# Optimization experiments

Measured on AMD Instinct MI355X. Metric: run time of the kernel, lower is better.

Reference implementation:

```python
import jax, jax.numpy as jnp
import numpy as np

HEAD_DIM = 128
PROJ_DIM = 64


def setup_inputs() -> dict:
    key = jax.random.key(0)
    kq, kk, kv, kr = jax.random.split(key, 4)
    B, H, NQ, NKV = 1, 16, 2048, 4096
    Q = jax.random.normal(kq, (B, H, NQ, HEAD_DIM), dtype=jnp.float32)
    K = jax.random.normal(kk, (B, H, NKV, HEAD_DIM), dtype=jnp.float32)
    V = jax.random.normal(kv, (B, H, NKV, HEAD_DIM), dtype=jnp.float32)
    # R ~ N(0,1) / sqrt(proj_dim), as in the torch __init__
    R = jax.random.normal(kr, (HEAD_DIM, PROJ_DIM), dtype=jnp.float32) / (PROJ_DIM ** 0.5)
    return {"Q": Q, "K": K, "V": V, "R": R}


def reference(Q, K, V, R):
    proj_dim = R.shape[-1]
    scale = 1.0 / (proj_dim ** 0.5)
    # Project Q and K into the random-projection space: [B,H,N,proj_dim]
    Q_proj = jnp.einsum('bhnd,dp->bhnp', Q, R)
    K_proj = jnp.einsum('bhmd,dp->bhmp', K, R)
    # scores: [B,H,NQ,NKV]
    scores = jnp.einsum('bhnp,bhmp->bhnm', Q_proj, K_proj) * scale
    weights = jax.nn.softmax(scores, axis=-1)
    # output: [B,H,NQ,head_dim]
    return jnp.einsum('bhnm,bhmd->bhnd', weights, V)
```

## Files before the change

kernel.cpp:

```cpp
#include <hip/hip_runtime.h>

#define HEADS 16
#define NQ    2048
#define NKV   4096
#define DH    128
#define PDIM  64

typedef __bf16 bf16_t;
typedef bf16_t bf16x8 __attribute__((ext_vector_type(8)));
typedef bf16_t bf16x4 __attribute__((ext_vector_type(4)));
typedef bf16_t bf16x2 __attribute__((ext_vector_type(2)));
typedef float  f32x4  __attribute__((ext_vector_type(4)));
typedef float  f32x16 __attribute__((ext_vector_type(16)));
typedef int    i32x4  __attribute__((ext_vector_type(4)));

typedef __attribute__((address_space(3))) unsigned int       lds_u32;
typedef __attribute__((address_space(1))) const unsigned int glb_u32;

__device__ __forceinline__ void dma16(const void* g, void* l) {
  __builtin_amdgcn_global_load_lds((glb_u32*)g, (lds_u32*)l, 16, 0, 0);
}

__global__ __launch_bounds__(256) void prep_kernel(
    const float* __restrict__ Q, const float* __restrict__ K,
    const float* __restrict__ V, const float* __restrict__ R,
    bf16_t* __restrict__ Qp, bf16_t* __restrict__ Kp, bf16_t* __restrict__ Vt)
{
  __shared__ float  sF[64 * 132];
  __shared__ bf16_t sY[4][16 * 72];
  const int tid = threadIdx.x;
  const int bid = blockIdx.x;

  const int isQ = (bid < 512);
  const int isK = (bid >= 512) && (bid < 1536);

  const float* src;
  long row0;
  if (isQ)      { src = Q; row0 = (long)bid * 64; }
  else if (isK) { src = K; row0 = (long)(bid - 512) * 64; }
  else          { src = V; row0 = (long)(bid - 1536) * 64; }
  const float* tp = src + row0 * DH;
#pragma unroll
  for (int rep = 0; rep < 8; ++rep) {
    const int slot = tid + rep * 256;
    const int j = slot >> 5, c4 = (slot & 31) * 4;
    f32x4 v = *(const f32x4*)(tp + j * DH + c4);
    *(f32x4*)(&sF[j * 132 + c4]) = v;
  }
  __syncthreads();

  if (!isQ && !isK) {
    const int vb = bid - 1536;
    const int h = vb >> 6, jt = vb & 63;
    bf16_t* op = Vt + (long)h * DH * NKV + jt * 64;
#pragma unroll
    for (int rep = 0; rep < 4; ++rep) {
      const int slot = tid + rep * 256;
      const int d = slot >> 3, j8 = (slot & 7) * 8;
      bf16x8 w;
#pragma unroll
      for (int jj = 0; jj < 8; ++jj) w[jj] = (bf16_t)sF[(j8 + jj) * 132 + d];
      *(bf16x8*)(op + (long)d * NKV + j8) = w;
    }
    return;
  }

  const int wave = tid >> 6, lane = tid & 63;
  const int n16  = lane & 15, quad = lane >> 4;
  const float scale = isQ ? 0.18033688011112042f : 1.0f;
  bf16_t* Y = isQ ? Qp : Kp;

  bf16x8 bfr[4][4];
#pragma unroll
  for (int nt = 0; nt < 4; ++nt) {
    const int n = nt * 16 + n16;
#pragma unroll
    for (int kk = 0; kk < 4; ++kk) {
      const int k0 = kk * 32 + quad * 8;
      bf16x8 b;
#pragma unroll
      for (int j = 0; j < 8; ++j) b[j] = (bf16_t)R[(k0 + j) * PDIM + n];
      bfr[nt][kk] = b;
    }
  }

  const int arow = wave * 16 + n16;
  bf16x8 a[4];
#pragma unroll
  for (int kk = 0; kk < 4; ++kk) {
    const int k0 = kk * 32 + quad * 8;
    f32x4 x0 = *(const f32x4*)(&sF[arow * 132 + k0]);
    f32x4 x1 = *(const f32x4*)(&sF[arow * 132 + k0 + 4]);
    bf16x8 av;
#pragma unroll
    for (int j = 0; j < 4; ++j) { av[j] = (bf16_t)(x0[j] * scale); av[4 + j] = (bf16_t)(x1[j] * scale); }
    a[kk] = av;
  }

  bf16_t* sy = sY[wave];
#pragma unroll
  for (int nt = 0; nt < 4; ++nt) {
    f32x4 acc = {0.f, 0.f, 0.f, 0.f};
#pragma unroll
    for (int kk = 0; kk < 4; ++kk)
      acc = __builtin_amdgcn_mfma_f32_16x16x32_bf16(a[kk], bfr[nt][kk], acc, 0, 0, 0);
#pragma unroll
    for (int r = 0; r < 4; ++r)
      sy[(quad * 4 + r) * 72 + nt * 16 + n16] = (bf16_t)acc[r];
  }
  const long xrow = row0 + wave * 16;
  const int row = lane >> 2, cg = lane & 3;
  bf16x8 w0 = *(const bf16x8*)(&sy[row * 72 + cg * 16]);
  bf16x8 w1 = *(const bf16x8*)(&sy[row * 72 + cg * 16 + 8]);
  *(bf16x8*)(Y + (xrow + row) * PDIM + cg * 16)     = w0;
  *(bf16x8*)(Y + (xrow + row) * PDIM + cg * 16 + 8) = w1;
}

__global__ __launch_bounds__(128, 2) void flash_kernel(
    const bf16_t* __restrict__ Qp, const bf16_t* __restrict__ Kp,
    const bf16_t* __restrict__ Vt, bf16_t* __restrict__ Opart,
    float* __restrict__ Lpart, float* __restrict__ Out,
    int splits, int iters)
{
  __shared__ char smem[24576];
  bf16_t* sK = (bf16_t*)smem;
  bf16_t* sV = (bf16_t*)(smem + 8192);

  const int tid  = threadIdx.x;
  const int wave = tid >> 6, lane = tid & 63;
  const int l31  = lane & 31, h = lane >> 5;

  const int head = blockIdx.x & 15;
  const int qt   = (blockIdx.x >> 4) & 15;
  const int sp   = blockIdx.x >> 8;

  const int qbase = qt * 128 + wave * 64;
  const int kv0   = sp * (64 * iters);

  bf16x8 qf[2][4];
#pragma unroll
  for (int qsub = 0; qsub < 2; ++qsub)
#pragma unroll
    for (int k = 0; k < 4; ++k)
      qf[qsub][k] = *(const bf16x8*)(Qp + ((long)head * NQ + qbase + qsub * 32 + l31) * PDIM
                                     + k * 16 + h * 8);

  f32x16 o[2][4] = {};
  float rsum[2] = {0.f, 0.f};

  const bf16_t* kpH = Kp + (long)head * NKV * PDIM;
  const bf16_t* vtH = Vt + (long)head * DH * NKV;

  const int sw = ((lane & 7) ^ ((lane >> 3) & 7)) * 8;
  const int r8 = lane >> 3;

  for (int t = 0; t < iters; ++t) {
    const int kvb = kv0 + t * 64;
    __syncthreads();
    if (wave == 0) {
#pragma unroll
      for (int i = 0; i < 8; ++i)
        dma16(kpH + (long)(kvb + i * 8 + r8) * PDIM + sw, smem + i * 1024);
#pragma unroll
      for (int i = 0; i < 4; ++i)
        dma16(vtH + (long)(i * 8 + r8) * NKV + kvb + sw, smem + 8192 + i * 1024);
    } else {
#pragma unroll
      for (int i = 4; i < 16; ++i)
        dma16(vtH + (long)(i * 8 + r8) * NKV + kvb + sw, smem + 8192 + i * 1024);
    }
    __syncthreads();

#pragma unroll
    for (int s = 0; s < 2; ++s) {
      int bfr[2][2][4];
#pragma unroll
      for (int qsub = 0; qsub < 2; ++qsub) {
        f32x16 sc = {};
        const int r = s * 32 + l31;
#pragma unroll
        for (int k = 0; k < 4; ++k) {
          const int c = 2 * k + h;
          const bf16x8 a = *(const bf16x8*)(sK + r * 64 + ((c ^ (r & 7)) * 8));
          sc = __builtin_amdgcn_mfma_f32_32x32x16_bf16(a, qf[qsub][k], sc, 0, 0, 0);
        }
        int pk[4][2];
#pragma unroll
        for (int rg = 0; rg < 4; ++rg) {
          const float p0 = __builtin_amdgcn_exp2f(sc[rg * 4 + 0]);
          const float p1 = __builtin_amdgcn_exp2f(sc[rg * 4 + 1]);
          const float p2 = __builtin_amdgcn_exp2f(sc[rg * 4 + 2]);
          const float p3 = __builtin_amdgcn_exp2f(sc[rg * 4 + 3]);
          rsum[qsub] += (p0 + p1) + (p2 + p3);
          union { bf16x2 v; int i; } u0, u1;
          u0.v = bf16x2{(bf16_t)p0, (bf16_t)p1};
          u1.v = bf16x2{(bf16_t)p2, (bf16_t)p3};
          pk[rg][0] = u0.i; pk[rg][1] = u1.i;
        }
#pragma unroll
        for (int cl = 0; cl < 2; ++cl) {
          const int e00 = __shfl_xor(pk[2 * cl][0], 32);
          const int e01 = __shfl_xor(pk[2 * cl][1], 32);
          const int e10 = __shfl_xor(pk[2 * cl + 1][0], 32);
          const int e11 = __shfl_xor(pk[2 * cl + 1][1], 32);
          bfr[qsub][cl][0] = h ? e10 : pk[2 * cl][0];
          bfr[qsub][cl][1] = h ? e11 : pk[2 * cl][1];
          bfr[qsub][cl][2] = h ? pk[2 * cl + 1][0] : e00;
          bfr[qsub][cl][3] = h ? pk[2 * cl + 1][1] : e01;
        }
      }
#pragma unroll
      for (int dsub = 0; dsub < 4; ++dsub) {
        const int r = dsub * 32 + l31;
#pragma unroll
        for (int cl = 0; cl < 2; ++cl) {
          const int c = 2 * (2 * s + cl) + h;
          const bf16x8 va = *(const bf16x8*)(sV + r * 64 + ((c ^ (r & 7)) * 8));
#pragma unroll
          for (int qsub = 0; qsub < 2; ++qsub) {
            union { i32x4 i; bf16x8 v; } pb;
            pb.i = i32x4{bfr[qsub][cl][0], bfr[qsub][cl][1],
                         bfr[qsub][cl][2], bfr[qsub][cl][3]};
            o[qsub][dsub] = __builtin_amdgcn_mfma_f32_32x32x16_bf16(va, pb.v, o[qsub][dsub], 0, 0, 0);
          }
        }
      }
    }
  }

  __syncthreads();
  bf16_t* myT = (bf16_t*)(smem + wave * 8704);
#pragma unroll
  for (int qsub = 0; qsub < 2; ++qsub) {
    const float lsum = rsum[qsub] + __shfl_xor(rsum[qsub], 32);
    const float scale = (splits > 1) ? 1.0f : (1.0f / lsum);
#pragma unroll
    for (int dsub = 0; dsub < 4; ++dsub)
#pragma unroll
      for (int rg = 0; rg < 4; ++rg) {
        bf16x4 w = { (bf16_t)(o[qsub][dsub][rg * 4 + 0] * scale),
                     (bf16_t)(o[qsub][dsub][rg * 4 + 1] * scale),
                     (bf16_t)(o[qsub][dsub][rg * 4 + 2] * scale),
                     (bf16_t)(o[qsub][dsub][rg * 4 + 3] * scale) };
        *(bf16x4*)(myT + l31 * 136 + dsub * 32 + rg * 8 + h * 4) = w;
      }
    const int qglob = qbase + qsub * 32;
#pragma unroll
    for (int j = 0; j < 8; ++j) {
      const int ql = j * 4 + (lane >> 4);
      bf16x8 v = *(const bf16x8*)(myT + ql * 136 + (lane & 15) * 8);
      if (splits > 1) {
        *(bf16x8*)(Opart + (((long)sp * HEADS + head) * NQ + qglob + ql) * DH + (lane & 15) * 8) = v;
      } else {
        float* op = Out + ((long)head * NQ + qglob + ql) * DH + (lane & 15) * 8;
        f32x4 a = {(float)v[0], (float)v[1], (float)v[2], (float)v[3]};
        f32x4 b = {(float)v[4], (float)v[5], (float)v[6], (float)v[7]};
        *(f32x4*)op = a; *(f32x4*)(op + 4) = b;
      }
    }
    if (splits > 1 && h == 0)
      Lpart[((long)sp * HEADS + head) * NQ + qglob + l31] = lsum;
  }
}

__global__ __launch_bounds__(256) void combine_kernel(
    const bf16_t* __restrict__ Opart, const float* __restrict__ Lpart,
    float* __restrict__ Out)
{
  const long idx = (long)blockIdx.x * 256 + threadIdx.x;
  const int  d8  = (int)(idx & 15);
  const long hq  = idx >> 4;
  float l = 0.f;
  float acc[8];
#pragma unroll
  for (int j = 0; j < 8; ++j) acc[j] = 0.f;
#pragma unroll
  for (int s = 0; s < 4; ++s) {
    l += Lpart[s * (long)(HEADS * NQ) + hq];
    bf16x8 v = *(const bf16x8*)(Opart + (s * (long)(HEADS * NQ) + hq) * DH + d8 * 8);
#pragma unroll
    for (int j = 0; j < 8; ++j) acc[j] += (float)v[j];
  }
  const float inv = 1.f / l;
  f32x4 o0 = { acc[0] * inv, acc[1] * inv, acc[2] * inv, acc[3] * inv };
  f32x4 o1 = { acc[4] * inv, acc[5] * inv, acc[6] * inv, acc[7] * inv };
  float* op = Out + hq * DH + d8 * 8;
  *(f32x4*)(op)     = o0;
  *(f32x4*)(op + 4) = o1;
}

extern "C" void kernel_launch(void* const* d_in, const int* in_sizes, int n_in,
                              void* d_out, int out_size, void* d_ws, size_t ws_size,
                              hipStream_t stream)
{
  const float* Q = (const float*)d_in[0];
  const float* K = (const float*)d_in[1];
  const float* V = (const float*)d_in[2];
  const float* R = (const float*)d_in[3];
  float* Out = (float*)d_out;

  char* ws = (char*)d_ws;
  bf16_t* Qp = (bf16_t*)(ws);
  bf16_t* Kp = (bf16_t*)(ws + (size_t)(4  << 20));
  bf16_t* Vt = (bf16_t*)(ws + (size_t)(12 << 20));
  bf16_t* Opart = (bf16_t*)(ws + (size_t)(28 << 20));
  float*  Lpart = (float*)(ws + (size_t)(60 << 20));

  const size_t need4 = (size_t)(60 << 20) + 4ull * HEADS * NQ * sizeof(float);
  const int splits = (ws_size >= need4) ? 4 : 1;
  const int iters  = NKV / (64 * splits);

  prep_kernel<<<2560, 256, 0, stream>>>(Q, K, V, R, Qp, Kp, Vt);
  flash_kernel<<<splits * 256, 128, 0, stream>>>(Qp, Kp, Vt, Opart, Lpart, Out,
                                                 splits, iters);
  if (splits == 4)
    combine_kernel<<<2048, 256, 0, stream>>>(Opart, Lpart, Out);
}
```

Measured before the change: 197.0 us.

## Double-buffer K/V tiles in flash kernel and use three KV splits

Replaces the single LDS buffer with two ping-pong buffers so the async global-to-LDS load of the next K/V tile overlaps with MFMA compute on the current one. The KV split count drops from four to three (768 blocks, about three per CU on 256 CUs), with uneven 22/21/21 tile partitions. The combine kernel now reduces three partials. This doubles LDS per block, which may limit occupancy, and changes workload balance across blocks.

```diff
diff --git a/kernel.cpp b/kernel.cpp
--- a/kernel.cpp
+++ b/kernel.cpp
@@ -119,12 +119,10 @@
 __global__ __launch_bounds__(128, 2) void flash_kernel(
     const bf16_t* __restrict__ Qp, const bf16_t* __restrict__ Kp,
     const bf16_t* __restrict__ Vt, bf16_t* __restrict__ Opart,
-    float* __restrict__ Lpart, float* __restrict__ Out,
-    int splits, int iters)
+    float* __restrict__ Lpart, float* __restrict__ Out, int splits)
 {
-  __shared__ char smem[24576];
-  bf16_t* sK = (bf16_t*)smem;
-  bf16_t* sV = (bf16_t*)(smem + 8192);
+  __shared__ char bufA[24576];
+  __shared__ char bufB[24576];
 
   const int tid  = threadIdx.x;
   const int wave = tid >> 6, lane = tid & 63;
@@ -135,7 +133,31 @@
   const int sp   = blockIdx.x >> 8;
 
   const int qbase = qt * 128 + wave * 64;
-  const int kv0   = sp * (64 * iters);
+  int n_t, t0;
+  if (splits == 3) { n_t = (sp == 0) ? 22 : 21; t0 = (sp == 0) ? 0 : 22 + 21 * (sp - 1); }
+  else             { n_t = 64; t0 = 0; }
+
+  const bf16_t* kpH = Kp + (long)head * NKV * PDIM;
+  const bf16_t* vtH = Vt + (long)head * DH * NKV;
+
+  const int sw = ((lane & 7) ^ ((lane >> 3) & 7)) * 8;
+  const int r8 = lane >> 3;
+
+  auto stage = [&](int t, char* buf) {
+    const int kvb = (t0 + t) * 64;
+    if (wave == 0) {
+#pragma unroll
+      for (int i = 0; i < 8; ++i)
+        dma16(kpH + (long)(kvb + i * 8 + r8) * PDIM + sw, buf + i * 1024);
+#pragma unroll
+      for (int i = 0; i < 4; ++i)
+        dma16(vtH + (long)(i * 8 + r8) * NKV + kvb + sw, buf + 8192 + i * 1024);
+    } else {
+#pragma unroll
+      for (int i = 4; i < 16; ++i)
+        dma16(vtH + (long)(i * 8 + r8) * NKV + kvb + sw, buf + 8192 + i * 1024);
+    }
+  };
 
   bf16x8 qf[2][4];
 #pragma unroll
@@ -148,29 +170,9 @@
   f32x16 o[2][4] = {};
   float rsum[2] = {0.f, 0.f};
 
-  const bf16_t* kpH = Kp + (long)head * NKV * PDIM;
-  const bf16_t* vtH = Vt + (long)head * DH * NKV;
-
-  const int sw = ((lane & 7) ^ ((lane >> 3) & 7)) * 8;
-  const int r8 = lane >> 3;
-
-  for (int t = 0; t < iters; ++t) {
-    const int kvb = kv0 + t * 64;
-    __syncthreads();
-    if (wave == 0) {
-#pragma unroll
-      for (int i = 0; i < 8; ++i)
-        dma16(kpH + (long)(kvb + i * 8 + r8) * PDIM + sw, smem + i * 1024);
-#pragma unroll
-      for (int i = 0; i < 4; ++i)
-        dma16(vtH + (long)(i * 8 + r8) * NKV + kvb + sw, smem + 8192 + i * 1024);
-    } else {
-#pragma unroll
-      for (int i = 4; i < 16; ++i)
-        dma16(vtH + (long)(i * 8 + r8) * NKV + kvb + sw, smem + 8192 + i * 1024);
-    }
-    __syncthreads();
-
+  auto compute = [&](const char* buf) {
+    const bf16_t* sK = (const bf16_t*)buf;
+    const bf16_t* sV = (const bf16_t*)(buf + 8192);
 #pragma unroll
     for (int s = 0; s < 2; ++s) {
       int bfr[2][2][4];
@@ -226,10 +228,21 @@
         }
       }
     }
+  };
+
+  stage(0, bufA);
+#pragma unroll 1
+  for (int t = 0; t < n_t; t += 2) {
+    __syncthreads();
+    if (t + 1 < n_t) stage(t + 1, bufB);
+    compute(bufA);
+    __syncthreads();
+    if (t + 2 < n_t) stage(t + 2, bufA);
+    if (t + 1 < n_t) compute(bufB);
   }
 
   __syncthreads();
-  bf16_t* myT = (bf16_t*)(smem + wave * 8704);
+  bf16_t* myT = (bf16_t*)(bufA + wave * 8704);
 #pragma unroll
   for (int qsub = 0; qsub < 2; ++qsub) {
     const float lsum = rsum[qsub] + __shfl_xor(rsum[qsub], 32);
@@ -275,7 +288,7 @@
 #pragma unroll
   for (int j = 0; j < 8; ++j) acc[j] = 0.f;
 #pragma unroll
-  for (int s = 0; s < 4; ++s) {
+  for (int s = 0; s < 3; ++s) {
     l += Lpart[s * (long)(HEADS * NQ) + hq];
     bf16x8 v = *(const bf16x8*)(Opart + (s * (long)(HEADS * NQ) + hq) * DH + d8 * 8);
 #pragma unroll
@@ -304,15 +317,13 @@
   bf16_t* Kp = (bf16_t*)(ws + (size_t)(4  << 20));
   bf16_t* Vt = (bf16_t*)(ws + (size_t)(12 << 20));
   bf16_t* Opart = (bf16_t*)(ws + (size_t)(28 << 20));
-  float*  Lpart = (float*)(ws + (size_t)(60 << 20));
-
-  const size_t need4 = (size_t)(60 << 20) + 4ull * HEADS * NQ * sizeof(float);
-  const int splits = (ws_size >= need4) ? 4 : 1;
-  const int iters  = NKV / (64 * splits);
+  float*  Lpart = (float*)(ws + (size_t)(52 << 20));
+
+  const size_t need3 = (size_t)(52 << 20) + 3ull * HEADS * NQ * sizeof(float);
+  const int splits = (ws_size >= need3) ? 3 : 1;
 
   prep_kernel<<<2560, 256, 0, stream>>>(Q, K, V, R, Qp, Kp, Vt);
-  flash_kernel<<<splits * 256, 128, 0, stream>>>(Qp, Kp, Vt, Opart, Lpart, Out,
-                                                 splits, iters);
-  if (splits == 4)
+  flash_kernel<<<splits * 256, 128, 0, stream>>>(Qp, Kp, Vt, Opart, Lpart, Out, splits);
+  if (splits == 3)
     combine_kernel<<<2048, 256, 0, stream>>>(Opart, Lpart, Out);
 }
```

Result: slower. 266.6 us (+35.4%).

## Split flash block into four waves of 32 query rows each

Applied to the files above, without the earlier changes.

The flash kernel moves from 2 waves with 64 query rows each to 4 waves with 32 rows each. Each block still covers 128 queries. Per-wave register use drops, since there is one set of Q fragments and accumulators instead of two, and the launch bound goes from (128,2) to (256,3). The K/V tile loads are now spread evenly across all four waves, and shared memory grows to hold a transpose buffer for each wave. In exchange, each K/V fragment read from LDS is reused by only one query subtile instead of two, which doubles LDS read traffic per MFMA.

```diff
diff --git a/kernel.cpp b/kernel.cpp
--- a/kernel.cpp
+++ b/kernel.cpp
@@ -116,13 +116,13 @@
   *(bf16x8*)(Y + (xrow + row) * PDIM + cg * 16 + 8) = w1;
 }
 
-__global__ __launch_bounds__(128, 2) void flash_kernel(
+__global__ __launch_bounds__(256, 3) void flash_kernel(
     const bf16_t* __restrict__ Qp, const bf16_t* __restrict__ Kp,
     const bf16_t* __restrict__ Vt, bf16_t* __restrict__ Opart,
     float* __restrict__ Lpart, float* __restrict__ Out,
     int splits, int iters)
 {
-  __shared__ char smem[24576];
+  __shared__ char smem[34816];
   bf16_t* sK = (bf16_t*)smem;
   bf16_t* sV = (bf16_t*)(smem + 8192);
 
@@ -134,95 +134,79 @@
   const int qt   = (blockIdx.x >> 4) & 15;
   const int sp   = blockIdx.x >> 8;
 
-  const int qbase = qt * 128 + wave * 64;
-  const int kv0   = sp * (64 * iters);
-
-  bf16x8 qf[2][4];
-#pragma unroll
-  for (int qsub = 0; qsub < 2; ++qsub)
-#pragma unroll
-    for (int k = 0; k < 4; ++k)
-      qf[qsub][k] = *(const bf16x8*)(Qp + ((long)head * NQ + qbase + qsub * 32 + l31) * PDIM
-                                     + k * 16 + h * 8);
-
-  f32x16 o[2][4] = {};
-  float rsum[2] = {0.f, 0.f};
+  const int qw   = qt * 128 + wave * 32;
+  const int kv0  = sp * (64 * iters);
 
   const bf16_t* kpH = Kp + (long)head * NKV * PDIM;
   const bf16_t* vtH = Vt + (long)head * DH * NKV;
 
   const int sw = ((lane & 7) ^ ((lane >> 3) & 7)) * 8;
   const int r8 = lane >> 3;
+
+  bf16x8 qf[4];
+#pragma unroll
+  for (int k = 0; k < 4; ++k)
+    qf[k] = *(const bf16x8*)(Qp + ((long)head * NQ + qw + l31) * PDIM + k * 16 + h * 8);
+
+  f32x16 o[4] = {};
+  float rsum = 0.f;
 
   for (int t = 0; t < iters; ++t) {
     const int kvb = kv0 + t * 64;
     __syncthreads();
-    if (wave == 0) {
-#pragma unroll
-      for (int i = 0; i < 8; ++i)
-        dma16(kpH + (long)(kvb + i * 8 + r8) * PDIM + sw, smem + i * 1024);
-#pragma unroll
-      for (int i = 0; i < 4; ++i)
-        dma16(vtH + (long)(i * 8 + r8) * NKV + kvb + sw, smem + 8192 + i * 1024);
-    } else {
-#pragma unroll
-      for (int i = 4; i < 16; ++i)
-        dma16(vtH + (long)(i * 8 + r8) * NKV + kvb + sw, smem + 8192 + i * 1024);
+#pragma unroll
+    for (int i = 0; i < 6; ++i) {
+      const int c = wave * 6 + i;
+      if (c < 8) dma16(kpH + (long)(kvb + c * 8 + r8) * PDIM + sw, smem + c * 1024);
+      else       dma16(vtH + (long)((c - 8) * 8 + r8) * NKV + kvb + sw, smem + c * 1024);
     }
     __syncthreads();
 
 #pragma unroll
     for (int s = 0; s < 2; ++s) {
-      int bfr[2][2][4];
-#pragma unroll
-      for (int qsub = 0; qsub < 2; ++qsub) {
-        f32x16 sc = {};
-        const int r = s * 32 + l31;
-#pragma unroll
-        for (int k = 0; k < 4; ++k) {
-          const int c = 2 * k + h;
-          const bf16x8 a = *(const bf16x8*)(sK + r * 64 + ((c ^ (r & 7)) * 8));
-          sc = __builtin_amdgcn_mfma_f32_32x32x16_bf16(a, qf[qsub][k], sc, 0, 0, 0);
-        }
-        int pk[4][2];
-#pragma unroll
-        for (int rg = 0; rg < 4; ++rg) {
-          const float p0 = __builtin_amdgcn_exp2f(sc[rg * 4 + 0]);
-          const float p1 = __builtin_amdgcn_exp2f(sc[rg * 4 + 1]);
-          const float p2 = __builtin_amdgcn_exp2f(sc[rg * 4 + 2]);
-          const float p3 = __builtin_amdgcn_exp2f(sc[rg * 4 + 3]);
-          rsum[qsub] += (p0 + p1) + (p2 + p3);
-          union { bf16x2 v; int i; } u0, u1;
-          u0.v = bf16x2{(bf16_t)p0, (bf16_t)p1};
-          u1.v = bf16x2{(bf16_t)p2, (bf16_t)p3};
-          pk[rg][0] = u0.i; pk[rg][1] = u1.i;
-        }
-#pragma unroll
-        for (int cl = 0; cl < 2; ++cl) {
-          const int e00 = __shfl_xor(pk[2 * cl][0], 32);
-          const int e01 = __shfl_xor(pk[2 * cl][1], 32);
-          const int e10 = __shfl_xor(pk[2 * cl + 1][0], 32);
-          const int e11 = __shfl_xor(pk[2 * cl + 1][1], 32);
-          bfr[qsub][cl][0] = h ? e10 : pk[2 * cl][0];
-          bfr[qsub][cl][1] = h ? e11 : pk[2 * cl][1];
-          bfr[qsub][cl][2] = h ? pk[2 * cl + 1][0] : e00;
-          bfr[qsub][cl][3] = h ? pk[2 * cl + 1][1] : e01;
-        }
+      f32x16 sc = {};
+      const int r = s * 32 + l31;
+#pragma unroll
+      for (int k = 0; k < 4; ++k) {
+        const int c = 2 * k + h;
+        const bf16x8 a = *(const bf16x8*)(sK + r * 64 + ((c ^ (r & 7)) * 8));
+        sc = __builtin_amdgcn_mfma_f32_32x32x16_bf16(a, qf[k], sc, 0, 0, 0);
+      }
+      int pk[4][2];
+#pragma unroll
+      for (int rg = 0; rg < 4; ++rg) {
+        const float p0 = __builtin_amdgcn_exp2f(sc[rg * 4 + 0]);
+        const float p1 = __builtin_amdgcn_exp2f(sc[rg * 4 + 1]);
+        const float p2 = __builtin_amdgcn_exp2f(sc[rg * 4 + 2]);
+        const float p3 = __builtin_amdgcn_exp2f(sc[rg * 4 + 3]);
+        rsum += (p0 + p1) + (p2 + p3);
+        union { bf16x2 v; int i; } u0, u1;
+        u0.v = bf16x2{(bf16_t)p0, (bf16_t)p1};
+        u1.v = bf16x2{(bf16_t)p2, (bf16_t)p3};
+        pk[rg][0] = u0.i; pk[rg][1] = u1.i;
+      }
+      int bfr[2][4];
+#pragma unroll
+      for (int cl = 0; cl < 2; ++cl) {
+        const int e00 = __shfl_xor(pk[2 * cl][0], 32);
+        const int e01 = __shfl_xor(pk[2 * cl][1], 32);
+        const int e10 = __shfl_xor(pk[2 * cl + 1][0], 32);
+        const int e11 = __shfl_xor(pk[2 * cl + 1][1], 32);
+        bfr[cl][0] = h ? e10 : pk[2 * cl][0];
+        bfr[cl][1] = h ? e11 : pk[2 * cl][1];
+        bfr[cl][2] = h ? pk[2 * cl + 1][0] : e00;
+        bfr[cl][3] = h ? pk[2 * cl + 1][1] : e01;
       }
 #pragma unroll
       for (int dsub = 0; dsub < 4; ++dsub) {
-        const int r = dsub * 32 + l31;
+        const int rv = dsub * 32 + l31;
 #pragma unroll
         for (int cl = 0; cl < 2; ++cl) {
           const int c = 2 * (2 * s + cl) + h;
-          const bf16x8 va = *(const bf16x8*)(sV + r * 64 + ((c ^ (r & 7)) * 8));
-#pragma unroll
-          for (int qsub = 0; qsub < 2; ++qsub) {
-            union { i32x4 i; bf16x8 v; } pb;
-            pb.i = i32x4{bfr[qsub][cl][0], bfr[qsub][cl][1],
-                         bfr[qsub][cl][2], bfr[qsub][cl][3]};
-            o[qsub][dsub] = __builtin_amdgcn_mfma_f32_32x32x16_bf16(va, pb.v, o[qsub][dsub], 0, 0, 0);
-          }
+          const bf16x8 va = *(const bf16x8*)(sV + rv * 64 + ((c ^ (rv & 7)) * 8));
+          union { i32x4 i; bf16x8 v; } pb;
+          pb.i = i32x4{bfr[cl][0], bfr[cl][1], bfr[cl][2], bfr[cl][3]};
+          o[dsub] = __builtin_amdgcn_mfma_f32_32x32x16_bf16(va, pb.v, o[dsub], 0, 0, 0);
         }
       }
     }
@@ -230,37 +214,33 @@
 
   __syncthreads();
   bf16_t* myT = (bf16_t*)(smem + wave * 8704);
-#pragma unroll
-  for (int qsub = 0; qsub < 2; ++qsub) {
-    const float lsum = rsum[qsub] + __shfl_xor(rsum[qsub], 32);
-    const float scale = (splits > 1) ? 1.0f : (1.0f / lsum);
-#pragma unroll
-    for (int dsub = 0; dsub < 4; ++dsub)
-#pragma unroll
-      for (int rg = 0; rg < 4; ++rg) {
-        bf16x4 w = { (bf16_t)(o[qsub][dsub][rg * 4 + 0] * scale),
-                     (bf16_t)(o[qsub][dsub][rg * 4 + 1] * scale),
-                     (bf16_t)(o[qsub][dsub][rg * 4 + 2] * scale),
-                     (bf16_t)(o[qsub][dsub][rg * 4 + 3] * scale) };
-        *(bf16x4*)(myT + l31 * 136 + dsub * 32 + rg * 8 + h * 4) = w;
-      }
-    const int qglob = qbase + qsub * 32;
-#pragma unroll
-    for (int j = 0; j < 8; ++j) {
-      const int ql = j * 4 + (lane >> 4);
-      bf16x8 v = *(const bf16x8*)(myT + ql * 136 + (lane & 15) * 8);
-      if (splits > 1) {
-        *(bf16x8*)(Opart + (((long)sp * HEADS + head) * NQ + qglob + ql) * DH + (lane & 15) * 8) = v;
-      } else {
-        float* op = Out + ((long)head * NQ + qglob + ql) * DH + (lane & 15) * 8;
-        f32x4 a = {(float)v[0], (float)v[1], (float)v[2], (float)v[3]};
-        f32x4 b = {(float)v[4], (float)v[5], (float)v[6], (float)v[7]};
-        *(f32x4*)op = a; *(f32x4*)(op + 4) = b;
-      }
-    }
-    if (splits > 1 && h == 0)
-      Lpart[((long)sp * HEADS + head) * NQ + qglob + l31] = lsum;
-  }
+  const float lsum = rsum + __shfl_xor(rsum, 32);
+  const float scale = (splits > 1) ? 1.0f : (1.0f / lsum);
+#pragma unroll
+  for (int dsub = 0; dsub < 4; ++dsub)
+#pragma unroll
+    for (int rg = 0; rg < 4; ++rg) {
+      bf16x4 w = { (bf16_t)(o[dsub][rg * 4 + 0] * scale),
+                   (bf16_t)(o[dsub][rg * 4 + 1] * scale),
+                   (bf16_t)(o[dsub][rg * 4 + 2] * scale),
+                   (bf16_t)(o[dsub][rg * 4 + 3] * scale) };
+      *(bf16x4*)(myT + l31 * 136 + dsub * 32 + rg * 8 + h * 4) = w;
+    }
+#pragma unroll
+  for (int j = 0; j < 8; ++j) {
+    const int ql = j * 4 + (lane >> 4);
+    bf16x8 v = *(const bf16x8*)(myT + ql * 136 + (lane & 15) * 8);
+    if (splits > 1) {
+      *(bf16x8*)(Opart + (((long)sp * HEADS + head) * NQ + qw + ql) * DH + (lane & 15) * 8) = v;
+    } else {
+      float* op = Out + ((long)head * NQ + qw + ql) * DH + (lane & 15) * 8;
+      f32x4 a = {(float)v[0], (float)v[1], (float)v[2], (float)v[3]};
+      f32x4 b = {(float)v[4], (float)v[5], (float)v[6], (float)v[7]};
+      *(f32x4*)op = a; *(f32x4*)(op + 4) = b;
+    }
+  }
+  if (splits > 1 && h == 0)
+    Lpart[((long)sp * HEADS + head) * NQ + qw + l31] = lsum;
 }
 
 __global__ __launch_bounds__(256) void combine_kernel(
@@ -311,7 +291,7 @@
   const int iters  = NKV / (64 * splits);
 
   prep_kernel<<<2560, 256, 0, stream>>>(Q, K, V, R, Qp, Kp, Vt);
-  flash_kernel<<<splits * 256, 128, 0, stream>>>(Qp, Kp, Vt, Opart, Lpart, Out,
+  flash_kernel<<<splits * 256, 256, 0, stream>>>(Qp, Kp, Vt, Opart, Lpart, Out,
                                                  splits, iters);
   if (splits == 4)
     combine_kernel<<<2048, 256, 0, stream>>>(Opart, Lpart, Out);
```

After: 205.1 us. 1.04x slower.
